# Optimization experiments

Hardware: AMD Instinct MI355X
Metric: run time of the kernel (lower is better)

Reference implementation:

```python
import jax, jax.numpy as jnp
import numpy as np

B = 256      # graph pairs
NPG = 28     # nodes per graph
MAXN = 32    # max_node_set_size
EPG = 64     # edges per graph (== max_edge_set_size, so no edge padding)
MAXE = 64
D = 128      # node_state_dim
FN = 32      # raw node feature dim
FE = 32      # raw edge feature dim
SK = 64      # sinkhorn_feature_dim
STEPS = 3    # propagation_steps
TEMP = 0.1
ITERS = 20
CW = 0.9     # consistency_weight
G = 2 * B
N = G * NPG
E = G * EPG


def _lin(key, fi, fo):
    return jax.random.normal(key, (fi, fo), jnp.float32) / np.sqrt(fi)


def setup_inputs() -> dict:
    key = jax.random.key(0)
    ks = jax.random.split(key, 12)
    rng = np.random.default_rng(0)
    off = (np.arange(G) * NPG)[:, None]   # graphs ordered q0,c0,q1,c1,...
    from_idx = jnp.asarray((rng.integers(0, NPG, (G, EPG)) + off).reshape(-1), jnp.int32)
    to_idx = jnp.asarray((rng.integers(0, NPG, (G, EPG)) + off).reshape(-1), jnp.int32)
    return dict(
        node_features=jax.random.normal(ks[0], (N, FN), jnp.float32),
        edge_features=jax.random.normal(ks[1], (E, FE), jnp.float32),
        enc_nw=_lin(ks[2], FN, D), enc_nb=jnp.zeros((D,), jnp.float32),
        enc_ew=_lin(ks[3], FE, D), enc_eb=jnp.zeros((D,), jnp.float32),
        msg_w1=_lin(ks[4], 3 * D, 2 * D), msg_b1=jnp.zeros((2 * D,), jnp.float32),
        msg_w2=_lin(ks[5], 2 * D, D), msg_b2=jnp.zeros((D,), jnp.float32),
        rmsg_w1=_lin(ks[6], 3 * D, 2 * D), rmsg_b1=jnp.zeros((2 * D,), jnp.float32),
        rmsg_w2=_lin(ks[7], 2 * D, D), rmsg_b2=jnp.zeros((D,), jnp.float32),
        upd_w1=_lin(ks[8], 2 * D, 2 * D), upd_b1=jnp.zeros((2 * D,), jnp.float32),
        upd_w2=_lin(ks[9], 2 * D, D), upd_b2=jnp.zeros((D,), jnp.float32),
        sk_w1=_lin(ks[10], D, SK), sk_b1=jnp.zeros((SK,), jnp.float32),
        sk_w2=_lin(ks[11], SK, SK), sk_b2=jnp.zeros((SK,), jnp.float32),
        from_idx=from_idx, to_idx=to_idx,
        query_sizes=jnp.full((B,), NPG, jnp.int32),
        corpus_sizes=jnp.full((B,), NPG, jnp.int32),
    )


def _mlp2(x, w1, b1, w2, b2):
    return jnp.maximum(x @ w1 + b1, 0.0) @ w2 + b2


def _sinkhorn(log_alpha):
    # log-domain sinkhorn (noise_factor = 0 -> deterministic)
    la = log_alpha / TEMP
    for _ in range(ITERS):
        la = la - jax.nn.logsumexp(la, axis=2, keepdims=True)
        la = la - jax.nn.logsumexp(la, axis=1, keepdims=True)
    return jnp.exp(la)


def _align(q, c, plan):
    # feature_alignment_score: -relu(q - P @ c).sum over set and feature dims
    return -jnp.maximum(q - plan @ c, 0.0).sum(axis=(1, 2))


def _forward(node_features, edge_features, enc_nw, enc_nb, enc_ew, enc_eb,
             msg_w1, msg_b1, msg_w2, msg_b2, rmsg_w1, rmsg_b1, rmsg_w2, rmsg_b2,
             upd_w1, upd_b1, upd_w2, upd_b2, sk_w1, sk_b1, sk_w2, sk_b2,
             from_idx, to_idx, query_sizes, corpus_sizes):
    h = node_features @ enc_nw + enc_nb        # encoder, [N, D]
    e = edge_features @ enc_ew + enc_eb        # [E, D]

    def messages(h):
        f = _mlp2(jnp.concatenate([h[from_idx], h[to_idx], e], -1), msg_w1, msg_b1, msg_w2, msg_b2)
        r = _mlp2(jnp.concatenate([h[to_idx], h[from_idx], e], -1), rmsg_w1, rmsg_b1, rmsg_w2, rmsg_b2)
        return f, r

    for _ in range(STEPS):  # GraphPropLayer x propagation_steps
        f, r = messages(h)
        agg = jax.ops.segment_sum(f, to_idx, num_segments=N) + \
              jax.ops.segment_sum(r, from_idx, num_segments=N)
        h = h + _mlp2(jnp.concatenate([agg, h], -1), upd_w1, upd_b1, upd_w2, upd_b2)

    # split_and_stack nodes: graphs alternate query/corpus, pad NPG -> MAXN
    hs = jnp.pad(h.reshape(B, 2, NPG, D), ((0, 0), (0, 0), (0, MAXN - NPG), (0, 0)))
    q_nodes, c_nodes = hs[:, 0], hs[:, 1]      # [B, MAXN, D]

    tq = _mlp2(q_nodes, sk_w1, sk_b1, sk_w2, sk_b2)
    tc = _mlp2(c_nodes, sk_w1, sk_b1, sk_w2, sk_b2)
    pos = jnp.arange(MAXN)[None, :]
    mq = tq * (pos < query_sizes[:, None])[..., None]
    mc = tc * (pos < corpus_sizes[:, None])[..., None]
    node_plan = _sinkhorn(jnp.einsum('bqd,bcd->bqc', mq, mc))   # [B, MAXN, MAXN]

    # propagation_messages on final node states
    f, r = messages(h)
    em = (f + r).reshape(B, 2, EPG, D)         # EPG == MAXE -> no pad
    q_edges, c_edges = em[:, 0], em[:, 1]

    # local (within-graph) endpoint indices for kronecker lookup
    fl = (from_idx % NPG).reshape(B, 2, EPG)
    tl = (to_idx % NPG).reshape(B, 2, EPG)
    qf, cf = fl[:, 0], fl[:, 1]
    qt, ct = tl[:, 0], tl[:, 1]

    def kron(T, qf, qt, cf, ct):
        straight = T[qf][:, cf] * T[qt][:, ct]   # [MAXE, MAXE]
        cross = T[qf][:, ct] * T[qt][:, cf]
        return straight + cross

    edge_scores = jax.vmap(kron)(node_plan, qf, qt, cf, ct)     # [B, MAXE, MAXE]
    edge_plan = _sinkhorn(edge_scores)

    return _align(q_nodes, c_nodes, node_plan) + CW * _align(q_edges, c_edges, edge_plan)


def reference(node_features, edge_features, enc_nw, enc_nb, enc_ew, enc_eb,
              msg_w1, msg_b1, msg_w2, msg_b2, rmsg_w1, rmsg_b1, rmsg_w2, rmsg_b2,
              upd_w1, upd_b1, upd_w2, upd_b2, sk_w1, sk_b1, sk_w2, sk_b2,
              from_idx, to_idx, query_sizes, corpus_sizes):
    return _forward(node_features, edge_features, enc_nw, enc_nb, enc_ew, enc_eb,
                    msg_w1, msg_b1, msg_w2, msg_b2, rmsg_w1, rmsg_b1, rmsg_w2, rmsg_b2,
                    upd_w1, upd_b1, upd_w2, upd_b2, sk_w1, sk_b1, sk_w2, sk_b2,
                    from_idx, to_idx, query_sizes, corpus_sizes)
```

## Files before the change

### kernel.cpp

```cpp
#include <hip/hip_runtime.h>
#include <math.h>

#define NPG 28
#define EPG 64
#define NB  256
#define NG  512
#define NN  14336
#define NE  32768
#define TEMPINV 10.0f
#define SINK_ITERS 20
#define CW 0.9f

typedef unsigned int uint;
typedef unsigned short ushort;
typedef __attribute__((ext_vector_type(8))) __bf16 bf16x8;
typedef __attribute__((ext_vector_type(4))) float f32x4;

__device__ __forceinline__ ushort f2bf(float x) {
    uint u = __float_as_uint(x);
    u += 0x7fffu + ((u >> 16) & 1u);
    return (ushort)(u >> 16);
}
__device__ __forceinline__ uint f2bf2(float lo, float hi) {
    return (uint)f2bf(lo) | ((uint)f2bf(hi) << 16);
}
__device__ __forceinline__ float bflo(uint w) { return __uint_as_float(w << 16); }
__device__ __forceinline__ float bfhi(uint w) { return __uint_as_float(w & 0xffff0000u); }
__device__ __forceinline__ uint relu_sum_pk(uint w1, uint w2, uint w3) {
    float lo = fmaxf(bflo(w1) + bflo(w2) + bflo(w3), 0.f);
    float hi = fmaxf(bfhi(w1) + bfhi(w2) + bfhi(w3), 0.f);
    return f2bf2(lo, hi);
}
__device__ __forceinline__ uint4 pack_f32x8(const float* src) {
    const float4 f0 = *(const float4*)src;
    const float4 f1 = *(const float4*)(src + 4);
    uint4 o;
    o.x = f2bf2(f0.x, f0.y);
    o.y = f2bf2(f0.z, f0.w);
    o.z = f2bf2(f1.x, f1.y);
    o.w = f2bf2(f1.z, f1.w);
    return o;
}
__device__ __forceinline__ f32x4 mfma16(bf16x8 a, bf16x8 b, f32x4 c) {
    return __builtin_amdgcn_mfma_f32_16x16x32_bf16(a, b, c, 0, 0, 0);
}

__global__ __launch_bounds__(512) void gnn_fused(
    const float* __restrict__ nf, const float* __restrict__ ef,
    const ushort* __restrict__ encL, const float* __restrict__ enc_nb,
    const ushort* __restrict__ WcombL, const float* __restrict__ bcomb,
    const ushort* __restrict__ WhpL,
    const ushort* __restrict__ W2fL, const ushort* __restrict__ W2rL,
    const float* __restrict__ b2f, const float* __restrict__ b2r,
    const ushort* __restrict__ UW1T, const float* __restrict__ ub1,
    const ushort* __restrict__ UW2T, const float* __restrict__ ub2,
    const int* __restrict__ from_idx, const int* __restrict__ to_idx,
    float* __restrict__ h, float* __restrict__ EM)
{
    __shared__ ushort HPs[NPG * 520];
    __shared__ ushort ECs[2 * 8 * 2048];
    __shared__ float acc_s[NPG * 132];
    __shared__ float hs[NPG * 132];
    __shared__ int fl[64], tl[64];
    const int g = blockIdx.x;
    const int tid = threadIdx.x;
    const int w = tid >> 6, lane = tid & 63;
    const int li = lane & 15, quad = lane >> 4;
    const int wm = w >> 1, wn = w & 1;
    ushort* hid = &HPs[0];

    if (tid < 64) {
        fl[tid] = from_idx[g * 64 + tid] - g * NPG;
        tl[tid] = to_idx[g * 64 + tid] - g * NPG;
    }

    {
        uint4 anf[2];
#pragma unroll
        for (int mi = 0; mi < 2; ++mi) {
            const int row = mi * 16 + li;
            const int rr = (row < NPG) ? row : 0;
            const float4 f0 = *(const float4*)(nf + ((size_t)g * NPG + rr) * 32 + quad * 8);
            const float4 f1 = *(const float4*)(nf + ((size_t)g * NPG + rr) * 32 + quad * 8 + 4);
            uint4 o;
            o.x = f2bf2(f0.x, f0.y); o.y = f2bf2(f0.z, f0.w);
            o.z = f2bf2(f1.x, f1.y); o.w = f2bf2(f1.z, f1.w);
            anf[mi] = o;
        }
        const int col = w * 16 + li;
        const bf16x8 b = __builtin_bit_cast(bf16x8,
            *(const uint4*)(encL + (size_t)col * 32 + quad * 8));
        f32x4 c0 = mfma16(__builtin_bit_cast(bf16x8, anf[0]), b, f32x4{0.f, 0.f, 0.f, 0.f});
        f32x4 c1 = mfma16(__builtin_bit_cast(bf16x8, anf[1]), b, f32x4{0.f, 0.f, 0.f, 0.f});
        const float bv = enc_nb[col];
#pragma unroll
        for (int r = 0; r < 4; ++r) {
            const int r0 = quad * 4 + r;
            hs[r0 * 132 + col] = c0[r] + bv;
            const int r1 = 16 + quad * 4 + r;
            if (r1 < NPG) hs[r1 * 132 + col] = c1[r] + bv;
        }
    }
    {
        uint4 aef[4];
#pragma unroll
        for (int mi = 0; mi < 4; ++mi) {
            const int e = mi * 16 + li;
            const float4 f0 = *(const float4*)(ef + ((size_t)g * 64 + e) * 32 + quad * 8);
            const float4 f1 = *(const float4*)(ef + ((size_t)g * 64 + e) * 32 + quad * 8 + 4);
            uint4 o;
            o.x = f2bf2(f0.x, f0.y); o.y = f2bf2(f0.z, f0.w);
            o.z = f2bf2(f1.x, f1.y); o.w = f2bf2(f1.z, f1.w);
            aef[mi] = o;
        }
#pragma unroll
        for (int ni = 0; ni < 4; ++ni) {
            const int col = w * 64 + ni * 16 + li;
            const bf16x8 b = __builtin_bit_cast(bf16x8,
                *(const uint4*)(WcombL + (size_t)col * 32 + quad * 8));
            const float bv = bcomb[col];
            const int pp = col >> 8, kbl = (col >> 5) & 7, j = col & 31;
#pragma unroll
            for (int mi = 0; mi < 4; ++mi) {
                f32x4 c = mfma16(__builtin_bit_cast(bf16x8, aef[mi]), b,
                                 f32x4{0.f, 0.f, 0.f, 0.f});
#pragma unroll
                for (int r = 0; r < 4; ++r) {
                    const int e = mi * 16 + quad * 4 + r;
                    ECs[pp * 16384 + kbl * 2048 + e * 32 + j] = f2bf(c[r] + bv);
                }
            }
        }
    }
    __syncthreads();

#pragma unroll 1
    for (int step = 0; step < 3; ++step) {
        uint4 ha[2][4];
#pragma unroll
        for (int mi = 0; mi < 2; ++mi) {
            const int row = mi * 16 + li;
            const int rr = (row < NPG) ? row : 0;
#pragma unroll
            for (int kb = 0; kb < 4; ++kb)
                ha[mi][kb] = pack_f32x8(&hs[rr * 132 + kb * 32 + quad * 8]);
        }
        for (int u = tid; u < NPG * 132; u += 512) acc_s[u] = 0.f;

        f32x4 acc[4];
#pragma unroll
        for (int j = 0; j < 4; ++j) acc[j] = f32x4{0.f, 0.f, 0.f, 0.f};

#pragma unroll 1
        for (int p = 0; p < 2; ++p) {
            {
                const int colw = w * 64;
#pragma unroll
                for (int ni = 0; ni < 4; ++ni) {
                    const int col = colw + ni * 16 + li;
                    const ushort* pb = WhpL + (size_t)(p * 512 + col) * 32 + quad * 8;
                    f32x4 c0 = f32x4{0.f, 0.f, 0.f, 0.f};
                    f32x4 c1 = f32x4{0.f, 0.f, 0.f, 0.f};
#pragma unroll
                    for (int kb = 0; kb < 4; ++kb) {
                        const bf16x8 b = __builtin_bit_cast(bf16x8,
                            *(const uint4*)(pb + (size_t)kb * 32768));
                        c0 = mfma16(__builtin_bit_cast(bf16x8, ha[0][kb]), b, c0);
                        c1 = mfma16(__builtin_bit_cast(bf16x8, ha[1][kb]), b, c1);
                    }
#pragma unroll
                    for (int r = 0; r < 4; ++r) {
                        const int r0 = quad * 4 + r;
                        HPs[r0 * 520 + col] = f2bf(c0[r]);
                        const int r1 = 16 + quad * 4 + r;
                        if (r1 < NPG) HPs[r1 * 520 + col] = f2bf(c1[r]);
                    }
                }
            }
            __syncthreads();

            if (p == 1) {
#pragma unroll
                for (int j = 0; j < 4; ++j) acc[j] = f32x4{0.f, 0.f, 0.f, 0.f};
            }
            const int e = wm * 16 + li;
            const int i1 = p ? tl[e] : fl[e];
            const int i2 = p ? fl[e] : tl[e];
            const int ad1 = i1 * 520 + quad * 8;
            const int ad2 = i2 * 520 + 256 + quad * 8;
            const int ade = p * 16384 + e * 32 + quad * 8;
            const ushort* W2L = p ? W2rL : W2fL;
            const int n0 = wn * 64;
            const ushort* pb[4];
#pragma unroll
            for (int ni = 0; ni < 4; ++ni)
                pb[ni] = W2L + (size_t)(n0 + ni * 16 + li) * 32 + quad * 8;
#pragma unroll
            for (int kb = 0; kb < 8; ++kb) {
                const uint4 u1 = *(const uint4*)&HPs[ad1 + kb * 32];
                const uint4 u2 = *(const uint4*)&HPs[ad2 + kb * 32];
                const uint4 ue = *(const uint4*)&ECs[ade + kb * 2048];
                uint4 o;
                o.x = relu_sum_pk(u1.x, u2.x, ue.x);
                o.y = relu_sum_pk(u1.y, u2.y, ue.y);
                o.z = relu_sum_pk(u1.z, u2.z, ue.z);
                o.w = relu_sum_pk(u1.w, u2.w, ue.w);
                const bf16x8 a = __builtin_bit_cast(bf16x8, o);
#pragma unroll
                for (int ni = 0; ni < 4; ++ni) {
                    const bf16x8 b = __builtin_bit_cast(bf16x8,
                        *(const uint4*)(pb[ni] + (size_t)kb * 4096));
                    acc[ni] = mfma16(a, b, acc[ni]);
                }
            }
            {
                const int* targ = p ? fl : tl;
                const float* bias = p ? b2r : b2f;
                float bv[4];
#pragma unroll
                for (int ni = 0; ni < 4; ++ni) bv[ni] = bias[n0 + ni * 16 + li];
#pragma unroll
                for (int r = 0; r < 4; ++r) {
                    const int loc = targ[wm * 16 + quad * 4 + r];
#pragma unroll
                    for (int ni = 0; ni < 4; ++ni)
                        atomicAdd(&acc_s[loc * 132 + n0 + ni * 16 + li],
                                  acc[ni][r] + bv[ni]);
                }
            }
            __syncthreads();
        }

        {
            const int n0u = w * 32;
            f32x4 ua[2][2];
#pragma unroll
            for (int mi = 0; mi < 2; ++mi)
#pragma unroll
                for (int ni = 0; ni < 2; ++ni) ua[mi][ni] = f32x4{0.f, 0.f, 0.f, 0.f};
            const ushort* pb0 = UW1T + (size_t)(n0u + li) * 256 + quad * 8;
            const ushort* pb1 = UW1T + (size_t)(n0u + 16 + li) * 256 + quad * 8;
#pragma unroll
            for (int kb = 0; kb < 8; ++kb) {
                bf16x8 a[2];
                if (kb < 4) {
#pragma unroll
                    for (int mi = 0; mi < 2; ++mi) {
                        const int row = mi * 16 + li;
                        const int rr = (row < NPG) ? row : 0;
                        a[mi] = __builtin_bit_cast(bf16x8,
                            pack_f32x8(&acc_s[rr * 132 + kb * 32 + quad * 8]));
                    }
                } else {
                    a[0] = __builtin_bit_cast(bf16x8, ha[0][kb - 4]);
                    a[1] = __builtin_bit_cast(bf16x8, ha[1][kb - 4]);
                }
                const bf16x8 b0 = __builtin_bit_cast(bf16x8, *(const uint4*)(pb0 + kb * 32));
                const bf16x8 b1 = __builtin_bit_cast(bf16x8, *(const uint4*)(pb1 + kb * 32));
#pragma unroll
                for (int mi = 0; mi < 2; ++mi) {
                    ua[mi][0] = mfma16(a[mi], b0, ua[mi][0]);
                    ua[mi][1] = mfma16(a[mi], b1, ua[mi][1]);
                }
            }
            const float bv0 = ub1[n0u + li], bv1 = ub1[n0u + 16 + li];
#pragma unroll
            for (int mi = 0; mi < 2; ++mi)
#pragma unroll
                for (int r = 0; r < 4; ++r) {
                    const int row = mi * 16 + quad * 4 + r;
                    if (row < NPG) {
                        hid[row * 264 + n0u + li] = f2bf(fmaxf(ua[mi][0][r] + bv0, 0.f));
                        hid[row * 264 + n0u + 16 + li] = f2bf(fmaxf(ua[mi][1][r] + bv1, 0.f));
                    }
                }
        }
        __syncthreads();
        {
            const int n0u = w * 16;
            f32x4 ua[2];
            ua[0] = f32x4{0.f, 0.f, 0.f, 0.f};
            ua[1] = f32x4{0.f, 0.f, 0.f, 0.f};
            const ushort* pb0 = UW2T + (size_t)(n0u + li) * 256 + quad * 8;
#pragma unroll
            for (int kb = 0; kb < 8; ++kb) {
                bf16x8 a[2];
#pragma unroll
                for (int mi = 0; mi < 2; ++mi) {
                    const int row = mi * 16 + li;
                    const int rr = (row < NPG) ? row : 0;
                    a[mi] = __builtin_bit_cast(bf16x8,
                        *(const uint4*)&hid[rr * 264 + kb * 32 + quad * 8]);
                }
                const bf16x8 b0 = __builtin_bit_cast(bf16x8, *(const uint4*)(pb0 + kb * 32));
                ua[0] = mfma16(a[0], b0, ua[0]);
                ua[1] = mfma16(a[1], b0, ua[1]);
            }
            const float bv = ub2[n0u + li];
#pragma unroll
            for (int mi = 0; mi < 2; ++mi)
#pragma unroll
                for (int r = 0; r < 4; ++r) {
                    const int row = mi * 16 + quad * 4 + r;
                    if (row < NPG)
                        hs[row * 132 + n0u + li] += ua[mi][r] + bv;
                }
        }
        __syncthreads();
    }

    {
        uint4 ha[2][4];
#pragma unroll
        for (int mi = 0; mi < 2; ++mi) {
            const int row = mi * 16 + li;
            const int rr = (row < NPG) ? row : 0;
#pragma unroll
            for (int kb = 0; kb < 4; ++kb)
                ha[mi][kb] = pack_f32x8(&hs[rr * 132 + kb * 32 + quad * 8]);
        }
        f32x4 acc[4];
#pragma unroll
        for (int j = 0; j < 4; ++j) acc[j] = f32x4{0.f, 0.f, 0.f, 0.f};
        const int n0 = wn * 64;
#pragma unroll 1
        for (int p = 0; p < 2; ++p) {
            {
                const int colw = w * 64;
#pragma unroll
                for (int ni = 0; ni < 4; ++ni) {
                    const int col = colw + ni * 16 + li;
                    const ushort* pb = WhpL + (size_t)(p * 512 + col) * 32 + quad * 8;
                    f32x4 c0 = f32x4{0.f, 0.f, 0.f, 0.f};
                    f32x4 c1 = f32x4{0.f, 0.f, 0.f, 0.f};
#pragma unroll
                    for (int kb = 0; kb < 4; ++kb) {
                        const bf16x8 b = __builtin_bit_cast(bf16x8,
                            *(const uint4*)(pb + (size_t)kb * 32768));
                        c0 = mfma16(__builtin_bit_cast(bf16x8, ha[0][kb]), b, c0);
                        c1 = mfma16(__builtin_bit_cast(bf16x8, ha[1][kb]), b, c1);
                    }
#pragma unroll
                    for (int r = 0; r < 4; ++r) {
                        const int r0 = quad * 4 + r;
                        HPs[r0 * 520 + col] = f2bf(c0[r]);
                        const int r1 = 16 + quad * 4 + r;
                        if (r1 < NPG) HPs[r1 * 520 + col] = f2bf(c1[r]);
                    }
                }
            }
            __syncthreads();
            const int e = wm * 16 + li;
            const int i1 = p ? tl[e] : fl[e];
            const int i2 = p ? fl[e] : tl[e];
            const int ad1 = i1 * 520 + quad * 8;
            const int ad2 = i2 * 520 + 256 + quad * 8;
            const int ade = p * 16384 + e * 32 + quad * 8;
            const ushort* W2L = p ? W2rL : W2fL;
            const ushort* pb[4];
#pragma unroll
            for (int ni = 0; ni < 4; ++ni)
                pb[ni] = W2L + (size_t)(n0 + ni * 16 + li) * 32 + quad * 8;
#pragma unroll
            for (int kb = 0; kb < 8; ++kb) {
                const uint4 u1 = *(const uint4*)&HPs[ad1 + kb * 32];
                const uint4 u2 = *(const uint4*)&HPs[ad2 + kb * 32];
                const uint4 ue = *(const uint4*)&ECs[ade + kb * 2048];
                uint4 o;
                o.x = relu_sum_pk(u1.x, u2.x, ue.x);
                o.y = relu_sum_pk(u1.y, u2.y, ue.y);
                o.z = relu_sum_pk(u1.z, u2.z, ue.z);
                o.w = relu_sum_pk(u1.w, u2.w, ue.w);
                const bf16x8 a = __builtin_bit_cast(bf16x8, o);
#pragma unroll
                for (int ni = 0; ni < 4; ++ni) {
                    const bf16x8 b = __builtin_bit_cast(bf16x8,
                        *(const uint4*)(pb[ni] + (size_t)kb * 4096));
                    acc[ni] = mfma16(a, b, acc[ni]);
                }
            }
            __syncthreads();
        }
        float bv[4];
#pragma unroll
        for (int ni = 0; ni < 4; ++ni)
            bv[ni] = b2f[n0 + ni * 16 + li] + b2r[n0 + ni * 16 + li];
#pragma unroll
        for (int r = 0; r < 4; ++r) {
            const int erow = g * 64 + wm * 16 + quad * 4 + r;
#pragma unroll
            for (int ni = 0; ni < 4; ++ni)
                EM[(size_t)erow * 128 + n0 + ni * 16 + li] = acc[ni][r] + bv[ni];
        }
    }
    for (int u = tid; u < NPG * 128; u += 512)
        h[(size_t)g * (NPG * 128) + u] = hs[(u >> 7) * 132 + (u & 127)];
}

__global__ __launch_bounds__(256) void pack2(
    const float* __restrict__ msg_w1, const float* __restrict__ rmsg_w1,
    const float* __restrict__ msg_b1, const float* __restrict__ rmsg_b1,
    const float* __restrict__ enc_ew, const float* __restrict__ enc_eb,
    const float* __restrict__ enc_nw,
    const float* __restrict__ msg_w2, const float* __restrict__ rmsg_w2,
    const float* __restrict__ upd_w1, const float* __restrict__ upd_w2,
    ushort* __restrict__ WcombL, float* __restrict__ bcomb,
    ushort* __restrict__ encL,
    ushort* __restrict__ WhpL, ushort* __restrict__ W2fL, ushort* __restrict__ W2rL,
    ushort* __restrict__ UW1T, ushort* __restrict__ UW2T)
{
    const int gid = blockIdx.x, tid = threadIdx.x;
    if (gid < 64) {
        const int idx = gid * 256 + tid;
        const int a = idx >> 9, n = idx & 511;
        const float* Wsrc = (n < 256) ? msg_w1 : rmsg_w1;
        const int nc = n & 255;
        float s = 0.f;
        for (int j = 0; j < 128; ++j)
            s = fmaf(enc_ew[a * 128 + j], Wsrc[(256 + j) * 256 + nc], s);
        WcombL[n * 32 + a] = f2bf(s);
    } else if (gid < 66) {
        const int n = (gid - 64) * 256 + tid;
        const float* Wsrc = (n < 256) ? msg_w1 : rmsg_w1;
        const float* bsrc = (n < 256) ? msg_b1 : rmsg_b1;
        const int nc = n & 255;
        float s = bsrc[nc];
        for (int j = 0; j < 128; ++j)
            s = fmaf(enc_eb[j], Wsrc[(256 + j) * 256 + nc], s);
        bcomb[n] = s;
    } else if (gid < 82) {
        const int idx = (gid - 66) * 256 + tid;
        const int n = idx >> 5, k = idx & 31;
        encL[idx] = f2bf(enc_nw[k * 128 + n]);
    } else if (gid < 594) {
        const int idx = (gid - 82) * 256 + tid;
        const int n = idx >> 7, k = idx & 127;
        const float* Wsrc = (n < 512) ? msg_w1 : rmsg_w1;
        const int part = (n >> 8) & 1, col = n & 255;
        WhpL[(size_t)(k >> 5) * 32768 + n * 32 + (k & 31)] =
            f2bf(Wsrc[(part * 128 + k) * 256 + col]);
    } else if (gid < 722) {
        const int idx = (gid - 594) * 256 + tid;
        const int n = idx >> 8, k = idx & 255;
        W2fL[(size_t)(k >> 5) * 4096 + n * 32 + (k & 31)] = f2bf(msg_w2[k * 128 + n]);
    } else if (gid < 850) {
        const int idx = (gid - 722) * 256 + tid;
        const int n = idx >> 8, k = idx & 255;
        W2rL[(size_t)(k >> 5) * 4096 + n * 32 + (k & 31)] = f2bf(rmsg_w2[k * 128 + n]);
    } else if (gid < 1106) {
        const int idx = (gid - 850) * 256 + tid;
        const int n = idx >> 8, k = idx & 255;
        UW1T[idx] = f2bf(upd_w1[k * 256 + n]);
    } else {
        const int idx = (gid - 1106) * 256 + tid;
        const int n = idx >> 8, k = idx & 255;
        UW2T[idx] = f2bf(upd_w2[k * 128 + n]);
    }
}

__global__ __launch_bounds__(256) void node_kernel(
    const float* __restrict__ h,
    const float* __restrict__ w1, const float* __restrict__ b1,
    const float* __restrict__ w2, const float* __restrict__ b2,
    const int* __restrict__ qsz, const int* __restrict__ csz,
    float* __restrict__ plan_out, float* __restrict__ loss_out)
{
    __shared__ float qn[32][128];
    __shared__ float cn[32][128];
    __shared__ float t1[32][64];
    __shared__ float mq[32][68];
    __shared__ float mc[32][68];
    __shared__ float la[32][33];
    __shared__ float red[4];
    const int bb = blockIdx.x;
    const int tid = threadIdx.x;
    const int qs = qsz[bb], cs = csz[bb];
    for (int u = tid * 4; u < 4096; u += 1024) {
        const int p = u >> 7, d = u & 127;
        float4 zq = make_float4(0.f, 0.f, 0.f, 0.f), zc = zq;
        if (p < NPG) {
            zq = *(const float4*)(h + (size_t)((2 * bb) * NPG + p) * 128 + d);
            zc = *(const float4*)(h + (size_t)((2 * bb + 1) * NPG + p) * 128 + d);
        }
        *(float4*)&qn[p][d] = zq;
        *(float4*)&cn[p][d] = zc;
    }
    __syncthreads();
    const int col = tid & 63;
    const int rg  = tid >> 6;
    for (int s = 0; s < 2; ++s) {
        const float (*src)[128] = s ? cn : qn;
        float (*dst)[68] = s ? mc : mq;
        const int sz = s ? cs : qs;
        float a8[8];
#pragma unroll
        for (int u = 0; u < 8; ++u) a8[u] = b1[col];
        for (int k = 0; k < 128; ++k) {
            const float wv = w1[k * 64 + col];
#pragma unroll
            for (int u = 0; u < 8; ++u) a8[u] = fmaf(src[rg + 4 * u][k], wv, a8[u]);
        }
#pragma unroll
        for (int u = 0; u < 8; ++u) t1[rg + 4 * u][col] = fmaxf(a8[u], 0.f);
        __syncthreads();
#pragma unroll
        for (int u = 0; u < 8; ++u) a8[u] = b2[col];
        for (int k = 0; k < 64; ++k) {
            const float wv = w2[k * 64 + col];
#pragma unroll
            for (int u = 0; u < 8; ++u) a8[u] = fmaf(t1[rg + 4 * u][k], wv, a8[u]);
        }
#pragma unroll
        for (int u = 0; u < 8; ++u) {
            const int r = rg + 4 * u;
            dst[r][col] = (r < sz) ? a8[u] : 0.f;
        }
        __syncthreads();
    }
    {
        const int q = tid >> 3, cg = tid & 7;
#pragma unroll
        for (int u = 0; u < 4; ++u) {
            const int c = cg + 8 * u;
            float s = 0.f;
            for (int d = 0; d < 64; ++d) s = fmaf(mq[q][d], mc[c][d], s);
            la[q][c] = s * TEMPINV;
        }
    }
    __syncthreads();
    const int l8 = tid & 7, rq = tid >> 3;
    for (int it = 0; it < SINK_ITERS; ++it) {
        {
            float x[4];
#pragma unroll
            for (int u = 0; u < 4; ++u) x[u] = la[rq][l8 * 4 + u];
            float m = fmaxf(fmaxf(x[0], x[1]), fmaxf(x[2], x[3]));
            m = fmaxf(m, __shfl_xor(m, 1));
            m = fmaxf(m, __shfl_xor(m, 2));
            m = fmaxf(m, __shfl_xor(m, 4));
            float s = __expf(x[0] - m) + __expf(x[1] - m) + __expf(x[2] - m) + __expf(x[3] - m);
            s += __shfl_xor(s, 1);
            s += __shfl_xor(s, 2);
            s += __shfl_xor(s, 4);
            const float lse = m + __logf(s);
#pragma unroll
            for (int u = 0; u < 4; ++u) la[rq][l8 * 4 + u] = x[u] - lse;
        }
        __syncthreads();
        {
            float x[4];
#pragma unroll
            for (int u = 0; u < 4; ++u) x[u] = la[l8 * 4 + u][rq];
            float m = fmaxf(fmaxf(x[0], x[1]), fmaxf(x[2], x[3]));
            m = fmaxf(m, __shfl_xor(m, 1));
            m = fmaxf(m, __shfl_xor(m, 2));
            m = fmaxf(m, __shfl_xor(m, 4));
            float s = __expf(x[0] - m) + __expf(x[1] - m) + __expf(x[2] - m) + __expf(x[3] - m);
            s += __shfl_xor(s, 1);
            s += __shfl_xor(s, 2);
            s += __shfl_xor(s, 4);
            const float lse = m + __logf(s);
#pragma unroll
            for (int u = 0; u < 4; ++u) la[l8 * 4 + u][rq] = x[u] - lse;
        }
        __syncthreads();
    }
    for (int u = tid; u < 1024; u += 256) {
        const int q = u >> 5, c = u & 31;
        const float p = __expf(la[q][c]);
        la[q][c] = p;
        plan_out[(size_t)bb * 1024 + u] = p;
    }
    __syncthreads();
    float lsum = 0.f;
    {
        const int q = tid >> 3, dg = tid & 7;
        for (int u = 0; u < 16; ++u) {
            const int d = dg + 8 * u;
            float pc = 0.f;
#pragma unroll
            for (int c = 0; c < 32; ++c) pc = fmaf(la[q][c], cn[c][d], pc);
            lsum += fmaxf(qn[q][d] - pc, 0.f);
        }
    }
#pragma unroll
    for (int off = 1; off < 64; off <<= 1) lsum += __shfl_xor(lsum, off);
    if ((tid & 63) == 0) red[tid >> 6] = lsum;
    __syncthreads();
    if (tid == 0) loss_out[bb] = -(red[0] + red[1] + red[2] + red[3]);
}

__global__ __launch_bounds__(256) void edge_kernel(
    const float* __restrict__ plan, const float* __restrict__ EM,
    const int* __restrict__ from_idx, const int* __restrict__ to_idx,
    float* __restrict__ loss_out)
{
    __shared__ float T[32][33];
    __shared__ float la[64][65];
    __shared__ float ce[64][128];
    __shared__ int qf[64], qt[64], cfi[64], cti[64];
    __shared__ float red[4];
    const int bb = blockIdx.x;
    const int tid = threadIdx.x;
    for (int u = tid; u < 1024; u += 256) T[u >> 5][u & 31] = plan[(size_t)bb * 1024 + u];
    if (tid < 64) {
        const int gq = 2 * bb, gc = 2 * bb + 1;
        qf[tid]  = from_idx[gq * 64 + tid] - gq * NPG;
        qt[tid]  = to_idx  [gq * 64 + tid] - gq * NPG;
        cfi[tid] = from_idx[gc * 64 + tid] - gc * NPG;
        cti[tid] = to_idx  [gc * 64 + tid] - gc * NPG;
    }
    {
        const int gc = 2 * bb + 1;
        for (int u = tid * 4; u < 8192; u += 1024) {
            const int i = u >> 7, d = u & 127;
            *(float4*)&ce[i][d] = *(const float4*)(EM + (size_t)(gc * 64 + i) * 128 + d);
        }
    }
    __syncthreads();
    {
        const int i = tid >> 2, jg = tid & 3;
        const int a = qf[i], b_ = qt[i];
#pragma unroll
        for (int u = 0; u < 16; ++u) {
            const int j = jg * 16 + u;
            const float s = T[a][cfi[j]] * T[b_][cti[j]] + T[a][cti[j]] * T[b_][cfi[j]];
            la[i][j] = s * TEMPINV;
        }
    }
    __syncthreads();
    const int l4 = tid & 3, rr = tid >> 2;
    for (int it = 0; it < SINK_ITERS; ++it) {
        {
            float x[16];
#pragma unroll
            for (int u = 0; u < 16; ++u) x[u] = la[rr][l4 * 16 + u];
            float m = x[0];
#pragma unroll
            for (int u = 1; u < 16; ++u) m = fmaxf(m, x[u]);
            m = fmaxf(m, __shfl_xor(m, 1));
            m = fmaxf(m, __shfl_xor(m, 2));
            float s = 0.f;
#pragma unroll
            for (int u = 0; u < 16; ++u) s += __expf(x[u] - m);
            s += __shfl_xor(s, 1);
            s += __shfl_xor(s, 2);
            const float lse = m + __logf(s);
#pragma unroll
            for (int u = 0; u < 16; ++u) la[rr][l4 * 16 + u] = x[u] - lse;
        }
        __syncthreads();
        {
            float x[16];
#pragma unroll
            for (int u = 0; u < 16; ++u) x[u] = la[l4 * 16 + u][rr];
            float m = x[0];
#pragma unroll
            for (int u = 1; u < 16; ++u) m = fmaxf(m, x[u]);
            m = fmaxf(m, __shfl_xor(m, 1));
            m = fmaxf(m, __shfl_xor(m, 2));
            float s = 0.f;
#pragma unroll
            for (int u = 0; u < 16; ++u) s += __expf(x[u] - m);
            s += __shfl_xor(s, 1);
            s += __shfl_xor(s, 2);
            const float lse = m + __logf(s);
#pragma unroll
            for (int u = 0; u < 16; ++u) la[l4 * 16 + u][rr] = x[u] - lse;
        }
        __syncthreads();
    }
    for (int u = tid; u < 4096; u += 256) la[u >> 6][u & 63] = __expf(la[u >> 6][u & 63]);
    __syncthreads();
    float lsum = 0.f;
    {
        const int q = tid >> 2, dg = tid & 3;
        const float* qe = EM + (size_t)((2 * bb) * 64 + q) * 128;
        for (int u = 0; u < 32; ++u) {
            const int d = dg + 4 * u;
            float pc = 0.f;
            for (int c = 0; c < 64; ++c) pc = fmaf(la[q][c], ce[c][d], pc);
            lsum += fmaxf(qe[d] - pc, 0.f);
        }
    }
#pragma unroll
    for (int off = 1; off < 64; off <<= 1) lsum += __shfl_xor(lsum, off);
    if ((tid & 63) == 0) red[tid >> 6] = lsum;
    __syncthreads();
    if (tid == 0) loss_out[bb] -= CW * (red[0] + red[1] + red[2] + red[3]);
}

extern "C" void kernel_launch(void* const* d_in, const int* in_sizes, int n_in,
                              void* d_out, int out_size, void* d_ws, size_t ws_size,
                              hipStream_t stream)
{
    const float* node_features = (const float*)d_in[0];
    const float* edge_features = (const float*)d_in[1];
    const float* enc_nw  = (const float*)d_in[2];
    const float* enc_nb  = (const float*)d_in[3];
    const float* enc_ew  = (const float*)d_in[4];
    const float* enc_eb  = (const float*)d_in[5];
    const float* msg_w1  = (const float*)d_in[6];
    const float* msg_b1  = (const float*)d_in[7];
    const float* msg_w2  = (const float*)d_in[8];
    const float* msg_b2  = (const float*)d_in[9];
    const float* rmsg_w1 = (const float*)d_in[10];
    const float* rmsg_b1 = (const float*)d_in[11];
    const float* rmsg_w2 = (const float*)d_in[12];
    const float* rmsg_b2 = (const float*)d_in[13];
    const float* upd_w1  = (const float*)d_in[14];
    const float* upd_b1  = (const float*)d_in[15];
    const float* upd_w2  = (const float*)d_in[16];
    const float* upd_b2  = (const float*)d_in[17];
    const float* sk_w1   = (const float*)d_in[18];
    const float* sk_b1   = (const float*)d_in[19];
    const float* sk_w2   = (const float*)d_in[20];
    const float* sk_b2   = (const float*)d_in[21];
    const int* from_idx  = (const int*)d_in[22];
    const int* to_idx    = (const int*)d_in[23];
    const int* qsizes    = (const int*)d_in[24];
    const int* csizes    = (const int*)d_in[25];
    float* out = (float*)d_out;

    float* ws     = (float*)d_ws;
    float* h      = ws;
    float* EM     = h + (size_t)NN * 128;
    float* plan   = EM + (size_t)NE * 128;
    float* bcomb  = plan + (size_t)NB * 1024;
    ushort* WcombL = (ushort*)(bcomb + 512);
    ushort* encL  = WcombL + 16384;
    ushort* WhpL  = encL + 4096;
    ushort* W2fL  = WhpL + 131072;
    ushort* W2rL  = W2fL + 32768;
    ushort* UW1T  = W2rL + 32768;
    ushort* UW2T  = UW1T + 65536;

    const dim3 blk(256);
    const dim3 blk512(512);

    pack2<<<1234, blk, 0, stream>>>(msg_w1, rmsg_w1, msg_b1, rmsg_b1,
                                    enc_ew, enc_eb, enc_nw, msg_w2, rmsg_w2,
                                    upd_w1, upd_w2,
                                    WcombL, bcomb, encL, WhpL, W2fL, W2rL, UW1T, UW2T);

    gnn_fused<<<dim3(NG), blk512, 0, stream>>>(
        node_features, edge_features, encL, enc_nb, WcombL, bcomb,
        WhpL, W2fL, W2rL, msg_b2, rmsg_b2,
        UW1T, upd_b1, UW2T, upd_b2, from_idx, to_idx, h, EM);

    node_kernel<<<NB, blk, 0, stream>>>(
        h, sk_w1, sk_b1, sk_w2, sk_b2, qsizes, csizes, plan, out);
    edge_kernel<<<NB, blk, 0, stream>>>(
        plan, EM, from_idx, to_idx, out);
}
```

Measured before the change: 468.9 us.

## Merge forward and reverse message passes into one projection and GEMM phase

```diff
diff --git a/kernel.cpp b/kernel.cpp
--- a/kernel.cpp
+++ b/kernel.cpp
@@ -44,6 +44,8 @@
 __device__ __forceinline__ f32x4 mfma16(bf16x8 a, bf16x8 b, f32x4 c) {
     return __builtin_amdgcn_mfma_f32_16x16x32_bf16(a, b, c, 0, 0, 0);
 }
+
+#define HP_STRIDE 1032
 
 __global__ __launch_bounds__(512) void gnn_fused(
     const float* __restrict__ nf, const float* __restrict__ ef,
@@ -57,7 +59,7 @@
     const int* __restrict__ from_idx, const int* __restrict__ to_idx,
     float* __restrict__ h, float* __restrict__ EM)
 {
-    __shared__ ushort HPs[NPG * 520];
+    __shared__ ushort HPs[NPG * HP_STRIDE];
     __shared__ ushort ECs[2 * 8 * 2048];
     __shared__ float acc_s[NPG * 132];
     __shared__ float hs[NPG * 132];
@@ -147,89 +149,107 @@
         }
         for (int u = tid; u < NPG * 132; u += 512) acc_s[u] = 0.f;
 
-        f32x4 acc[4];
-#pragma unroll
-        for (int j = 0; j < 4; ++j) acc[j] = f32x4{0.f, 0.f, 0.f, 0.f};
-
-#pragma unroll 1
-        for (int p = 0; p < 2; ++p) {
+        {
+            const int cw = w * 128;
+#pragma unroll
+            for (int ni = 0; ni < 8; ++ni) {
+                const int c = cw + ni * 16 + li;
+                const ushort* pb = WhpL + (size_t)c * 32 + quad * 8;
+                f32x4 c0 = f32x4{0.f, 0.f, 0.f, 0.f};
+                f32x4 c1 = f32x4{0.f, 0.f, 0.f, 0.f};
+#pragma unroll
+                for (int kb = 0; kb < 4; ++kb) {
+                    const bf16x8 b = __builtin_bit_cast(bf16x8,
+                        *(const uint4*)(pb + (size_t)kb * 32768));
+                    c0 = mfma16(__builtin_bit_cast(bf16x8, ha[0][kb]), b, c0);
+                    c1 = mfma16(__builtin_bit_cast(bf16x8, ha[1][kb]), b, c1);
+                }
+#pragma unroll
+                for (int r = 0; r < 4; ++r) {
+                    const int r0 = quad * 4 + r;
+                    HPs[r0 * HP_STRIDE + c] = f2bf(c0[r]);
+                    const int r1 = 16 + quad * 4 + r;
+                    if (r1 < NPG) HPs[r1 * HP_STRIDE + c] = f2bf(c1[r]);
+                }
+            }
+        }
+        __syncthreads();
+
+        {
+            const int e = wm * 16 + li;
+            const int fe = fl[e], te = tl[e];
+            const int adf1 = fe * HP_STRIDE + quad * 8;
+            const int adf2 = te * HP_STRIDE + 256 + quad * 8;
+            const int adr1 = te * HP_STRIDE + 512 + quad * 8;
+            const int adr2 = fe * HP_STRIDE + 768 + quad * 8;
+            const int adef = e * 32 + quad * 8;
+            const int ader = 16384 + e * 32 + quad * 8;
+            const int n0 = wn * 64;
+            const ushort* pbf[4];
+            const ushort* pbr[4];
+#pragma unroll
+            for (int ni = 0; ni < 4; ++ni) {
+                pbf[ni] = W2fL + (size_t)(n0 + ni * 16 + li) * 32 + quad * 8;
+                pbr[ni] = W2rL + (size_t)(n0 + ni * 16 + li) * 32 + quad * 8;
+            }
+            f32x4 accf[4], accr[4];
+#pragma unroll
+            for (int j = 0; j < 4; ++j) {
+                accf[j] = f32x4{0.f, 0.f, 0.f, 0.f};
+                accr[j] = f32x4{0.f, 0.f, 0.f, 0.f};
+            }
+#pragma unroll
+            for (int kb = 0; kb < 8; ++kb) {
+                const uint4 uf1 = *(const uint4*)&HPs[adf1 + kb * 32];
+                const uint4 uf2 = *(const uint4*)&HPs[adf2 + kb * 32];
+                const uint4 uef = *(const uint4*)&ECs[adef + kb * 2048];
+                const uint4 ur1 = *(const uint4*)&HPs[adr1 + kb * 32];
+                const uint4 ur2 = *(const uint4*)&HPs[adr2 + kb * 32];
+                const uint4 uer = *(const uint4*)&ECs[ader + kb * 2048];
+                uint4 of, orr;
+                of.x = relu_sum_pk(uf1.x, uf2.x, uef.x);
+                of.y = relu_sum_pk(uf1.y, uf2.y, uef.y);
+                of.z = relu_sum_pk(uf1.z, uf2.z, uef.z);
+                of.w = relu_sum_pk(uf1.w, uf2.w, uef.w);
+                orr.x = relu_sum_pk(ur1.x, ur2.x, uer.x);
+                orr.y = relu_sum_pk(ur1.y, ur2.y, uer.y);
+                orr.z = relu_sum_pk(ur1.z, ur2.z, uer.z);
+                orr.w = relu_sum_pk(ur1.w, ur2.w, uer.w);
+                const bf16x8 af = __builtin_bit_cast(bf16x8, of);
+                const bf16x8 ar = __builtin_bit_cast(bf16x8, orr);
+#pragma unroll
+                for (int ni = 0; ni < 4; ++ni) {
+                    const bf16x8 bf = __builtin_bit_cast(bf16x8,
+                        *(const uint4*)(pbf[ni] + (size_t)kb * 4096));
+                    const bf16x8 br = __builtin_bit_cast(bf16x8,
+                        *(const uint4*)(pbr[ni] + (size_t)kb * 4096));
+                    accf[ni] = mfma16(af, bf, accf[ni]);
+                    accr[ni] = mfma16(ar, br, accr[ni]);
+                }
+            }
             {
-                const int colw = w * 64;
+                float bvf[4], bvr[4];
 #pragma unroll
                 for (int ni = 0; ni < 4; ++ni) {
-                    const int col = colw + ni * 16 + li;
-                    const ushort* pb = WhpL + (size_t)(p * 512 + col) * 32 + quad * 8;
-                    f32x4 c0 = f32x4{0.f, 0.f, 0.f, 0.f};
-                    f32x4 c1 = f32x4{0.f, 0.f, 0.f, 0.f};
-#pragma unroll
-                    for (int kb = 0; kb < 4; ++kb) {
-                        const bf16x8 b = __builtin_bit_cast(bf16x8,
-                            *(const uint4*)(pb + (size_t)kb * 32768));
-                        c0 = mfma16(__builtin_bit_cast(bf16x8, ha[0][kb]), b, c0);
-                        c1 = mfma16(__builtin_bit_cast(bf16x8, ha[1][kb]), b, c1);
+                    bvf[ni] = b2f[n0 + ni * 16 + li];
+                    bvr[ni] = b2r[n0 + ni * 16 + li];
+                }
+#pragma unroll
+                for (int r = 0; r < 4; ++r) {
+                    const int er = wm * 16 + quad * 4 + r;
+                    const int locf = tl[er];
+                    const int locr = fl[er];
+#pragma unroll
+                    for (int ni = 0; ni < 4; ++ni) {
+                        atomicAdd(&acc_s[locf * 132 + n0 + ni * 16 + li],
+                                  accf[ni][r] + bvf[ni]);
+                        atomicAdd(&acc_s[locr * 132 + n0 + ni * 16 + li],
+                                  accr[ni][r] + bvr[ni]);
                     }
-#pragma unroll
-                    for (int r = 0; r < 4; ++r) {
-                        const int r0 = quad * 4 + r;
-                        HPs[r0 * 520 + col] = f2bf(c0[r]);
-                        const int r1 = 16 + quad * 4 + r;
-                        if (r1 < NPG) HPs[r1 * 520 + col] = f2bf(c1[r]);
-                    }
-                }
-            }
-            __syncthreads();
-
-            if (p == 1) {
-#pragma unroll
-                for (int j = 0; j < 4; ++j) acc[j] = f32x4{0.f, 0.f, 0.f, 0.f};
-            }
-            const int e = wm * 16 + li;
-            const int i1 = p ? tl[e] : fl[e];
-            const int i2 = p ? fl[e] : tl[e];
-            const int ad1 = i1 * 520 + quad * 8;
-            const int ad2 = i2 * 520 + 256 + quad * 8;
-            const int ade = p * 16384 + e * 32 + quad * 8;
-            const ushort* W2L = p ? W2rL : W2fL;
-            const int n0 = wn * 64;
-            const ushort* pb[4];
-#pragma unroll
-            for (int ni = 0; ni < 4; ++ni)
-                pb[ni] = W2L + (size_t)(n0 + ni * 16 + li) * 32 + quad * 8;
-#pragma unroll
-            for (int kb = 0; kb < 8; ++kb) {
-                const uint4 u1 = *(const uint4*)&HPs[ad1 + kb * 32];
-                const uint4 u2 = *(const uint4*)&HPs[ad2 + kb * 32];
-                const uint4 ue = *(const uint4*)&ECs[ade + kb * 2048];
-                uint4 o;
-                o.x = relu_sum_pk(u1.x, u2.x, ue.x);
-                o.y = relu_sum_pk(u1.y, u2.y, ue.y);
-                o.z = relu_sum_pk(u1.z, u2.z, ue.z);
-                o.w = relu_sum_pk(u1.w, u2.w, ue.w);
-                const bf16x8 a = __builtin_bit_cast(bf16x8, o);
-#pragma unroll
-                for (int ni = 0; ni < 4; ++ni) {
-                    const bf16x8 b = __builtin_bit_cast(bf16x8,
-                        *(const uint4*)(pb[ni] + (size_t)kb * 4096));
-                    acc[ni] = mfma16(a, b, acc[ni]);
-                }
-            }
-            {
-                const int* targ = p ? fl : tl;
-                const float* bias = p ? b2r : b2f;
-                float bv[4];
-#pragma unroll
-                for (int ni = 0; ni < 4; ++ni) bv[ni] = bias[n0 + ni * 16 + li];
-#pragma unroll
-                for (int r = 0; r < 4; ++r) {
-                    const int loc = targ[wm * 16 + quad * 4 + r];
-#pragma unroll
-                    for (int ni = 0; ni < 4; ++ni)
-                        atomicAdd(&acc_s[loc * 132 + n0 + ni * 16 + li],
-                                  acc[ni][r] + bv[ni]);
-                }
-            }
-            __syncthreads();
-        }
+                }
+            }
+        }
+        __syncthreads();
 
         {
             const int n0u = w * 32;
@@ -319,78 +339,95 @@
             for (int kb = 0; kb < 4; ++kb)
                 ha[mi][kb] = pack_f32x8(&hs[rr * 132 + kb * 32 + quad * 8]);
         }
-        f32x4 acc[4];
-#pragma unroll
-        for (int j = 0; j < 4; ++j) acc[j] = f32x4{0.f, 0.f, 0.f, 0.f};
-        const int n0 = wn * 64;
-#pragma unroll 1
-        for (int p = 0; p < 2; ++p) {
-            {
-                const int colw = w * 64;
+        {
+            const int cw = w * 128;
+#pragma unroll
+            for (int ni = 0; ni < 8; ++ni) {
+                const int c = cw + ni * 16 + li;
+                const ushort* pb = WhpL + (size_t)c * 32 + quad * 8;
+                f32x4 c0 = f32x4{0.f, 0.f, 0.f, 0.f};
+                f32x4 c1 = f32x4{0.f, 0.f, 0.f, 0.f};
+#pragma unroll
+                for (int kb = 0; kb < 4; ++kb) {
+                    const bf16x8 b = __builtin_bit_cast(bf16x8,
+                        *(const uint4*)(pb + (size_t)kb * 32768));
+                    c0 = mfma16(__builtin_bit_cast(bf16x8, ha[0][kb]), b, c0);
+                    c1 = mfma16(__builtin_bit_cast(bf16x8, ha[1][kb]), b, c1);
+                }
+#pragma unroll
+                for (int r = 0; r < 4; ++r) {
+                    const int r0 = quad * 4 + r;
+                    HPs[r0 * HP_STRIDE + c] = f2bf(c0[r]);
+                    const int r1 = 16 + quad * 4 + r;
+                    if (r1 < NPG) HPs[r1 * HP_STRIDE + c] = f2bf(c1[r]);
+                }
+            }
+        }
+        __syncthreads();
+        {
+            const int e = wm * 16 + li;
+            const int fe = fl[e], te = tl[e];
+            const int adf1 = fe * HP_STRIDE + quad * 8;
+            const int adf2 = te * HP_STRIDE + 256 + quad * 8;
+            const int adr1 = te * HP_STRIDE + 512 + quad * 8;
+            const int adr2 = fe * HP_STRIDE + 768 + quad * 8;
+            const int adef = e * 32 + quad * 8;
+            const int ader = 16384 + e * 32 + quad * 8;
+            const int n0 = wn * 64;
+            const ushort* pbf[4];
+            const ushort* pbr[4];
+#pragma unroll
+            for (int ni = 0; ni < 4; ++ni) {
+                pbf[ni] = W2fL + (size_t)(n0 + ni * 16 + li) * 32 + quad * 8;
+                pbr[ni] = W2rL + (size_t)(n0 + ni * 16 + li) * 32 + quad * 8;
+            }
+            f32x4 accf[4], accr[4];
+#pragma unroll
+            for (int j = 0; j < 4; ++j) {
+                accf[j] = f32x4{0.f, 0.f, 0.f, 0.f};
+                accr[j] = f32x4{0.f, 0.f, 0.f, 0.f};
+            }
+#pragma unroll
+            for (int kb = 0; kb < 8; ++kb) {
+                const uint4 uf1 = *(const uint4*)&HPs[adf1 + kb * 32];
+                const uint4 uf2 = *(const uint4*)&HPs[adf2 + kb * 32];
+                const uint4 uef = *(const uint4*)&ECs[adef + kb * 2048];
+                const uint4 ur1 = *(const uint4*)&HPs[adr1 + kb * 32];
+                const uint4 ur2 = *(const uint4*)&HPs[adr2 + kb * 32];
+                const uint4 uer = *(const uint4*)&ECs[ader + kb * 2048];
+                uint4 of, orr;
+                of.x = relu_sum_pk(uf1.x, uf2.x, uef.x);
+                of.y = relu_sum_pk(uf1.y, uf2.y, uef.y);
+                of.z = relu_sum_pk(uf1.z, uf2.z, uef.z);
+                of.w = relu_sum_pk(uf1.w, uf2.w, uef.w);
+                orr.x = relu_sum_pk(ur1.x, ur2.x, uer.x);
+                orr.y = relu_sum_pk(ur1.y, ur2.y, uer.y);
+                orr.z = relu_sum_pk(ur1.z, ur2.z, uer.z);
+                orr.w = relu_sum_pk(ur1.w, ur2.w, uer.w);
+                const bf16x8 af = __builtin_bit_cast(bf16x8, of);
+                const bf16x8 ar = __builtin_bit_cast(bf16x8, orr);
 #pragma unroll
                 for (int ni = 0; ni < 4; ++ni) {
-                    const int col = colw + ni * 16 + li;
-                    const ushort* pb = WhpL + (size_t)(p * 512 + col) * 32 + quad * 8;
-                    f32x4 c0 = f32x4{0.f, 0.f, 0.f, 0.f};
-                    f32x4 c1 = f32x4{0.f, 0.f, 0.f, 0.f};
-#pragma unroll
-                    for (int kb = 0; kb < 4; ++kb) {
-                        const bf16x8 b = __builtin_bit_cast(bf16x8,
-                            *(const uint4*)(pb + (size_t)kb * 32768));
-                        c0 = mfma16(__builtin_bit_cast(bf16x8, ha[0][kb]), b, c0);
-                        c1 = mfma16(__builtin_bit_cast(bf16x8, ha[1][kb]), b, c1);
-                    }
-#pragma unroll
-                    for (int r = 0; r < 4; ++r) {
-                        const int r0 = quad * 4 + r;
-                        HPs[r0 * 520 + col] = f2bf(c0[r]);
-                        const int r1 = 16 + quad * 4 + r;
-                        if (r1 < NPG) HPs[r1 * 520 + col] = f2bf(c1[r]);
-                    }
-                }
-            }
-            __syncthreads();
-            const int e = wm * 16 + li;
-            const int i1 = p ? tl[e] : fl[e];
-            const int i2 = p ? fl[e] : tl[e];
-            const int ad1 = i1 * 520 + quad * 8;
-            const int ad2 = i2 * 520 + 256 + quad * 8;
-            const int ade = p * 16384 + e * 32 + quad * 8;
-            const ushort* W2L = p ? W2rL : W2fL;
-            const ushort* pb[4];
+                    const bf16x8 bf = __builtin_bit_cast(bf16x8,
+                        *(const uint4*)(pbf[ni] + (size_t)kb * 4096));
+                    const bf16x8 br = __builtin_bit_cast(bf16x8,
+                        *(const uint4*)(pbr[ni] + (size_t)kb * 4096));
+                    accf[ni] = mfma16(af, bf, accf[ni]);
+                    accr[ni] = mfma16(ar, br, accr[ni]);
+                }
+            }
+            float bv[4];
 #pragma unroll
             for (int ni = 0; ni < 4; ++ni)
-                pb[ni] = W2L + (size_t)(n0 + ni * 16 + li) * 32 + quad * 8;
-#pragma unroll
-            for (int kb = 0; kb < 8; ++kb) {
-                const uint4 u1 = *(const uint4*)&HPs[ad1 + kb * 32];
-                const uint4 u2 = *(const uint4*)&HPs[ad2 + kb * 32];
-                const uint4 ue = *(const uint4*)&ECs[ade + kb * 2048];
-                uint4 o;
-                o.x = relu_sum_pk(u1.x, u2.x, ue.x);
-                o.y = relu_sum_pk(u1.y, u2.y, ue.y);
-                o.z = relu_sum_pk(u1.z, u2.z, ue.z);
-                o.w = relu_sum_pk(u1.w, u2.w, ue.w);
-                const bf16x8 a = __builtin_bit_cast(bf16x8, o);
-#pragma unroll
-                for (int ni = 0; ni < 4; ++ni) {
-                    const bf16x8 b = __builtin_bit_cast(bf16x8,
-                        *(const uint4*)(pb[ni] + (size_t)kb * 4096));
-                    acc[ni] = mfma16(a, b, acc[ni]);
-                }
-            }
-            __syncthreads();
-        }
-        float bv[4];
-#pragma unroll
-        for (int ni = 0; ni < 4; ++ni)
-            bv[ni] = b2f[n0 + ni * 16 + li] + b2r[n0 + ni * 16 + li];
-#pragma unroll
-        for (int r = 0; r < 4; ++r) {
-            const int erow = g * 64 + wm * 16 + quad * 4 + r;
-#pragma unroll
-            for (int ni = 0; ni < 4; ++ni)
-                EM[(size_t)erow * 128 + n0 + ni * 16 + li] = acc[ni][r] + bv[ni];
+                bv[ni] = b2f[n0 + ni * 16 + li] + b2r[n0 + ni * 16 + li];
+#pragma unroll
+            for (int r = 0; r < 4; ++r) {
+                const int erow = g * 64 + wm * 16 + quad * 4 + r;
+#pragma unroll
+                for (int ni = 0; ni < 4; ++ni)
+                    EM[(size_t)erow * 128 + n0 + ni * 16 + li] =
+                        accf[ni][r] + accr[ni][r] + bv[ni];
+            }
         }
     }
     for (int u = tid; u < NPG * 128; u += 512)
```

After: 884.1 us. +88.5%, slower.
